# Kernel tuning notes

Hardware: AMD Instinct MI355X
Metric: run time of the kernel (lower is better)

## Reference

```python
import jax, jax.numpy as jnp
import numpy as np

N_SKILLS = 1000
N_PROBLEMS = 20000
EMB = 256
TIME_LOG = 5.0
B, S = 32, 2048


def setup_inputs() -> dict:
    key = jax.random.key(0)
    ks = jax.random.split(key, 10)
    skills = jax.random.randint(ks[0], (B, S), 0, N_SKILLS, dtype=jnp.int64) if jax.config.jax_enable_x64 else jax.random.randint(ks[0], (B, S), 0, N_SKILLS, dtype=jnp.int32)
    problems = jax.random.randint(ks[1], (B, S), 0, N_PROBLEMS, dtype=skills.dtype)
    times = jnp.sort(jax.random.randint(ks[2], (B, S), 0, 10_000_000, dtype=skills.dtype), axis=-1)
    labels = jax.random.randint(ks[3], (B, S), 0, 2, dtype=skills.dtype)
    std = 0.01
    alpha_inter_W = std * jax.random.normal(ks[4], (2 * N_SKILLS, EMB), dtype=jnp.float32)
    alpha_skill_W = std * jax.random.normal(ks[5], (N_SKILLS, EMB), dtype=jnp.float32)
    beta_inter_W = std * jax.random.normal(ks[6], (2 * N_SKILLS, EMB), dtype=jnp.float32)
    beta_skill_W = std * jax.random.normal(ks[7], (N_SKILLS, EMB), dtype=jnp.float32)
    problem_base_W = std * jax.random.normal(ks[8], (N_PROBLEMS, 1), dtype=jnp.float32)
    skill_base_W = std * jax.random.normal(ks[9], (N_SKILLS, 1), dtype=jnp.float32)
    return {
        "skills": skills, "problems": problems, "times": times, "labels": labels,
        "alpha_inter_W": alpha_inter_W, "alpha_skill_W": alpha_skill_W,
        "beta_inter_W": beta_inter_W, "beta_skill_W": beta_skill_W,
        "problem_base_W": problem_base_W, "skill_base_W": skill_base_W,
    }


def reference(skills, problems, times, labels,
              alpha_inter_W, alpha_skill_W, beta_inter_W, beta_skill_W,
              problem_base_W, skill_base_W):
    n_skills = alpha_skill_W.shape[0]
    inters = skills + labels * n_skills  # [B,S]

    alpha_src = alpha_inter_W[inters]      # [B,S,E]
    alpha_tgt = alpha_skill_W[skills]      # [B,S,E]
    alphas = jnp.einsum("bse,bte->bst", alpha_src, alpha_tgt)  # [B,S,S]

    beta_src = beta_inter_W[inters]
    beta_tgt = beta_skill_W[skills]
    betas = jnp.einsum("bse,bte->bst", beta_src, beta_tgt)
    betas = jnp.clip(betas + 1.0, 0.0, 10.0)

    t = times.astype(jnp.float32) / 1000.0
    delta_t = jnp.abs(t[:, :, None] - t[:, None, :])
    delta_t = jnp.log(delta_t + 1e-10) / jnp.log(jnp.float32(TIME_LOG))

    cross = alphas * jnp.exp(-betas * delta_t)  # [B,S,S]

    seq_len = skills.shape[1]
    # original keeps strict upper triangle (source i strictly before target j)
    keep = jnp.triu(jnp.ones((seq_len, seq_len), dtype=cross.dtype), k=1)
    sum_t = jnp.sum(cross * keep[None], axis=-2)  # sum over source dim -> [B,S]

    problem_bias = problem_base_W[problems][..., 0]  # [B,S]
    skill_bias = skill_base_W[skills][..., 0]        # [B,S]
    h = problem_bias + skill_bias + sum_t
    return jax.nn.sigmoid(h)
```

## Files before the change

kernel.cpp:

```cpp
#include <hip/hip_runtime.h>
#include <hip/hip_bf16.h>
#include <stdint.h>

#define NSK   1000
#define EMB   256
#define BB    32
#define SS    2048
#define TI    128
#define TJ    64
#define NUNITB 272
#define BK    64
#define NCHUNK (EMB / BK)
#define LDSB  24576
#define SCALE_INV (1.0f / 4096.0f)
#define LOG5I 0.6213349345596119f

typedef float f32x16 __attribute__((ext_vector_type(16)));
typedef float f32x4  __attribute__((ext_vector_type(4)));
typedef long  longx2 __attribute__((ext_vector_type(2)));
typedef int   i32x8  __attribute__((ext_vector_type(8)));

#define OFF_AI8 0
#define OFF_BI8 (2 * NSK * EMB)
#define OFF_AS8 (4 * NSK * EMB)
#define OFF_BS8 (5 * NSK * EMB)
#define TOT8    (6 * NSK * EMB)

__global__ void cvt_tables(const float* __restrict__ ai, const float* __restrict__ bi,
                           const float* __restrict__ as_, const float* __restrict__ bs,
                           int* __restrict__ ws8, float* __restrict__ acc) {
    int g = blockIdx.x * 256 + threadIdx.x;
    if (g < BB * SS) acc[g] = 0.0f;
    if (g * 4 >= TOT8) return;
    int e = g * 4;
    const float* src; int off;
    if (e < OFF_AS8) { if (e < OFF_BI8) { src = ai;  off = e; }
                       else             { src = bi;  off = e - OFF_BI8; } }
    else             { if (e < OFF_BS8) { src = as_; off = e - OFF_AS8; }
                       else             { src = bs;  off = e - OFF_BS8; } }
    const float4 v = *(const float4*)(src + off);
    int lo = __builtin_amdgcn_cvt_pk_fp8_f32(v.x * 64.0f, v.y * 64.0f, 0, false);
    int wd = __builtin_amdgcn_cvt_pk_fp8_f32(v.z * 64.0f, v.w * 64.0f, lo, true);
    ws8[g] = wd;
}

__device__ __attribute__((noinline)) float dot256(const float* __restrict__ a,
                                                  const float* __restrict__ b) {
    float s = 0.0f;
#pragma unroll 8
    for (int k = 0; k < EMB; ++k) s += a[k] * b[k];
    return s;
}

__global__ __launch_bounds__(256, 3) void hawkes_unit(
    const int* __restrict__ skills, const int* __restrict__ times,
    const int* __restrict__ labels, const unsigned char* __restrict__ tab,
    const float* __restrict__ aiW_f, const float* __restrict__ asW_f,
    const float* __restrict__ biW_f, const float* __restrict__ bsW_f,
    float* __restrict__ acc)
{
    __shared__ __align__(16) char  sbuf[2 * LDSB];
    __shared__ __align__(16) float t_i[TI];
    __shared__ __align__(16) float t_j[TJ];
    __shared__ int   idx_i[TI];
    __shared__ int   idx_j[TJ];
    __shared__ float colsum[TJ];

    const int u  = blockIdx.x;
    const int b  = u / NUNITB;
    const int p  = u - b * NUNITB;
    int m = (int)sqrtf((float)p);
    while ((m + 1) * (m + 2) <= p) ++m;
    while (m * (m + 1) > p) --m;
    int jt, it;
    if (p >= (m + 1) * (m + 1)) { jt = 2 * m + 1; it = p - (m + 1) * (m + 1); }
    else                        { jt = 2 * m;     it = p - m * (m + 1); }
    const int j0 = jt * TJ, i0 = it * TI;
    const bool partial = (i0 + TI - 1 >= j0);

    const int tid = threadIdx.x;
    const int l   = tid & 63;
    const int w   = tid >> 6;
    const int wi  = w >> 1, wj = w & 1;
    const int lane31 = l & 31;
    const int khalf  = l >> 5;

    if (tid < TJ) {
        int j = j0 + tid;
        idx_j[tid] = skills[b * SS + j];
        t_j[tid]   = (float)times[b * SS + j] / 1000.0f;
        colsum[tid] = 0.0f;
    } else if (tid < TJ + TI) {
        int q = tid - TJ;
        int ii = i0 + q;
        idx_i[q] = skills[b * SS + ii] + labels[b * SS + ii] * NSK;
        t_i[q]   = (float)times[b * SS + ii] / 1000.0f;
    }
    __syncthreads();

    const float tjv = t_j[wj * 32 + lane31];
    const int   jl  = wj * 32 + lane31;

    const unsigned char* rowptr[3];
    int wo[3];
#pragma unroll
    for (int s = 0; s < 3; ++s) {
        int mm = w * 3 + s;
        int tabbase, ldsbase, row;
        if (mm < 8) {
            int mb = mm & 3;
            tabbase = (mm < 4) ? OFF_AI8 : OFF_BI8;
            ldsbase = ((mm < 4) ? 0 : 8192) + mb * 2048;
            row = idx_i[mb * 32 + (l >> 1)];
        } else {
            int mb = mm & 1;
            tabbase = (mm < 10) ? OFF_AS8 : OFF_BS8;
            ldsbase = ((mm < 10) ? 16384 : 20480) + mb * 2048;
            row = idx_j[mb * 32 + (l >> 1)];
        }
        rowptr[s] = tab + tabbase + (size_t)row * EMB + (l & 1) * 32;
        wo[s] = ldsbase + (l & 1) * 1024 + (l >> 1) * 8;
    }

#define LOADC(dst, c)                                                  \
    do { _Pragma("unroll")                                             \
        for (int s = 0; s < 3; ++s) {                                  \
            dst[s][0] = *(const longx2*)(rowptr[s] + (c) * BK);        \
            dst[s][1] = *(const longx2*)(rowptr[s] + (c) * BK + 16);   \
        }                                                              \
    } while (0)
#define WRITEC(src, buf)                                               \
    do { char* db = sbuf + (buf) * LDSB;                               \
        _Pragma("unroll")                                              \
        for (int s = 0; s < 3; ++s) {                                  \
            *(long*)(db + wo[s])             = src[s][0].x;            \
            *(long*)(db + wo[s] + 256)       = src[s][0].y;            \
            *(long*)(db + wo[s] + 512)       = src[s][1].x;            \
            *(long*)(db + wo[s] + 512 + 256) = src[s][1].y;            \
        }                                                              \
    } while (0)

    f32x16 accA[2], accB[2];
#pragma unroll
    for (int mi = 0; mi < 2; ++mi) { accA[mi] = 0.0f; accB[mi] = 0.0f; }

    longx2 sreg[3][2];
    LOADC(sreg, 0);
    WRITEC(sreg, 0);

    union U8 { long l[4]; i32x8 v; };

    for (int c = 0; c < NCHUNK; ++c) {
        if (c + 1 < NCHUNK) LOADC(sreg, c + 1);
        __syncthreads();

        const char* sb = sbuf + (c & 1) * LDSB;
        {
            U8 F0, F1, G;
#pragma unroll
            for (int q = 0; q < 4; ++q) {
                const int qoff = (khalf * 2 + (q >> 1)) * 512 + (q & 1) * 256 + lane31 * 8;
                F0.l[q] = *(const long*)(sb + 0 + (wi * 2 + 0) * 2048 + qoff);
                F1.l[q] = *(const long*)(sb + 0 + (wi * 2 + 1) * 2048 + qoff);
                G.l[q]  = *(const long*)(sb + 16384 + wj * 2048 + qoff);
            }
            accA[0] = __builtin_amdgcn_mfma_scale_f32_32x32x64_f8f6f4(
                F0.v, G.v, accA[0], 0, 0, 0, 127, 0, 127);
            accA[1] = __builtin_amdgcn_mfma_scale_f32_32x32x64_f8f6f4(
                F1.v, G.v, accA[1], 0, 0, 0, 127, 0, 127);
        }
        {
            U8 F0, F1, G;
#pragma unroll
            for (int q = 0; q < 4; ++q) {
                const int qoff = (khalf * 2 + (q >> 1)) * 512 + (q & 1) * 256 + lane31 * 8;
                F0.l[q] = *(const long*)(sb + 8192 + (wi * 2 + 0) * 2048 + qoff);
                F1.l[q] = *(const long*)(sb + 8192 + (wi * 2 + 1) * 2048 + qoff);
                G.l[q]  = *(const long*)(sb + 20480 + wj * 2048 + qoff);
            }
            accB[0] = __builtin_amdgcn_mfma_scale_f32_32x32x64_f8f6f4(
                F0.v, G.v, accB[0], 0, 0, 0, 127, 0, 127);
            accB[1] = __builtin_amdgcn_mfma_scale_f32_32x32x64_f8f6f4(
                F1.v, G.v, accB[1], 0, 0, 0, 127, 0, 127);
        }

        if (c + 1 < NCHUNK) WRITEC(sreg, (c + 1) & 1);
    }

    float csum0 = 0.0f, csum1 = 0.0f;
    float dmin = 1.0f;
#pragma unroll
    for (int mi = 0; mi < 2; ++mi) {
        const int rbase = (wi * 2 + mi) * 32 + 4 * khalf;
        f32x4 tiv[4];
#pragma unroll
        for (int q = 0; q < 4; ++q) tiv[q] = *(const f32x4*)(t_i + rbase + 8 * q);
        if (!partial) {
#pragma unroll
            for (int r = 0; r < 16; ++r) {
                const int q = r >> 2, e = r & 3;
                float d  = fabsf(tiv[q][e] - tjv);
                float lg = __builtin_amdgcn_logf(d);
                lg = (d == 0.0f) ? 1.0e38f : lg;
                dmin = fminf(dmin, d);
                float bp  = __builtin_fmaf(accB[mi][r], SCALE_INV * LOG5I, LOG5I);
                float wgt = __builtin_amdgcn_exp2f(-bp * lg);
                if (r & 1) csum1 = __builtin_fmaf(accA[mi][r], wgt, csum1);
                else       csum0 = __builtin_fmaf(accA[mi][r], wgt, csum0);
            }
        } else {
#pragma unroll
            for (int r = 0; r < 16; ++r) {
                const int q = r >> 2, e = r & 3;
                const int il = rbase + 8 * q + e;
                const bool live = (i0 + il < j0 + jl);
                float d  = fabsf(tiv[q][e] - tjv);
                float lg = __builtin_amdgcn_logf(d);
                lg = (d == 0.0f) ? 1.0e38f : lg;
                dmin = live ? fminf(dmin, d) : dmin;
                float bp  = __builtin_fmaf(accB[mi][r], SCALE_INV * LOG5I, LOG5I);
                float a   = live ? accA[mi][r] : 0.0f;
                float wgt = __builtin_amdgcn_exp2f(-bp * lg);
                if (r & 1) csum1 = __builtin_fmaf(a, wgt, csum1);
                else       csum0 = __builtin_fmaf(a, wgt, csum0);
            }
        }
    }
    float csum = csum0 + csum1;

    if (__any(dmin == 0.0f)) {
        const float dl0 = __builtin_amdgcn_logf(1e-10f) * LOG5I;
        for (int mi = 0; mi < 2; ++mi) {
            const int rbase = (wi * 2 + mi) * 32 + 4 * khalf;
            for (int r = 0; r < 16; ++r) {
                const int il = rbase + 8 * (r >> 2) + (r & 3);
                if (partial && i0 + il >= j0 + jl) continue;
                if (fabsf(t_i[il] - tjv) == 0.0f) {
                    float alpha = dot256(aiW_f + (size_t)idx_i[il] * EMB,
                                         asW_f + (size_t)idx_j[jl] * EMB) * 4096.0f;
                    float braw  = dot256(biW_f + (size_t)idx_i[il] * EMB,
                                         bsW_f + (size_t)idx_j[jl] * EMB) * 4096.0f;
                    float beta = braw * SCALE_INV + 1.0f;
                    csum += alpha * __builtin_amdgcn_exp2f(-beta * dl0);
                }
            }
        }
    }
    csum *= SCALE_INV;

    __syncthreads();
    csum += __shfl_xor(csum, 32);
    if (l < 32)
        atomicAdd(&colsum[wj * 32 + lane31], csum);
    __syncthreads();
    if (tid < TJ)
        atomicAdd(&acc[b * SS + j0 + tid], colsum[tid]);
}

__global__ void hawkes_final(const int* __restrict__ skills, const int* __restrict__ problems,
                             const float* __restrict__ pbW, const float* __restrict__ sbW,
                             float* __restrict__ out) {
    int i = blockIdx.x * 256 + threadIdx.x;
    if (i >= BB * SS) return;
    float h = pbW[problems[i]] + sbW[skills[i]] + out[i];
    out[i] = 1.0f / (1.0f + __builtin_amdgcn_exp2f(-h * 1.4426950408889634f));
}

extern "C" void kernel_launch(void* const* d_in, const int* in_sizes, int n_in,
                              void* d_out, int out_size, void* d_ws, size_t ws_size,
                              hipStream_t stream) {
    const int*   skills   = (const int*)d_in[0];
    const int*   problems = (const int*)d_in[1];
    const int*   times    = (const int*)d_in[2];
    const int*   labels   = (const int*)d_in[3];
    const float* aiW      = (const float*)d_in[4];
    const float* asW      = (const float*)d_in[5];
    const float* biW      = (const float*)d_in[6];
    const float* bsW      = (const float*)d_in[7];
    const float* pbW      = (const float*)d_in[8];
    const float* sbW      = (const float*)d_in[9];
    float* out = (float*)d_out;
    unsigned char* tab = (unsigned char*)d_ws;

    cvt_tables<<<(TOT8 / 4 + 255) / 256, 256, 0, stream>>>(aiW, biW, asW, bsW,
                                                           (int*)tab, out);
    hawkes_unit<<<BB * NUNITB, 256, 0, stream>>>(skills, times, labels, tab,
                                                 aiW, asW, biW, bsW, out);
    hawkes_final<<<(BB * SS + 255) / 256, 256, 0, stream>>>(skills, problems, pbW, sbW, out);
}
```

Baseline: 164.0 us.

## Stage fp8 embedding tiles via direct global-to-LDS loads with new fragment layout

Replaces the register-staged global load plus LDS store of the fp8 embedding rows with the global_load_lds builtin (16 bytes per lane), writing straight into the double-buffered LDS tile. The LDS layout changes so each MFMA fragment is read with two 16-byte LDS loads instead of four 8-byte ones. This is meant to cut VGPR pressure and the LDS write instructions, and to overlap the next chunk's fetch with compute. It relies on the implicit lane-contiguous LDS placement of global_load_lds matching the new fragment offsets, and on the existing barrier being enough to order the asynchronous LDS writes.

```diff
diff --git a/kernel.cpp b/kernel.cpp
--- a/kernel.cpp
+++ b/kernel.cpp
@@ -52,6 +52,12 @@
     return s;
 }
 
+#define GLL(gp, lp)                                                        \
+    __builtin_amdgcn_global_load_lds(                                      \
+        (const __attribute__((address_space(1))) unsigned int*)(const void*)(gp), \
+        (__attribute__((address_space(3))) unsigned int*)(void*)(lp),      \
+        16, 0, 0)
+
 __global__ __launch_bounds__(256, 3) void hawkes_unit(
     const int* __restrict__ skills, const int* __restrict__ times,
     const int* __restrict__ labels, const unsigned char* __restrict__ tab,
@@ -101,8 +107,8 @@
     const float tjv = t_j[wj * 32 + lane31];
     const int   jl  = wj * 32 + lane31;
 
-    const unsigned char* rowptr[3];
-    int wo[3];
+    const unsigned char* rowbase[3];
+    int ldso[3];
 #pragma unroll
     for (int s = 0; s < 3; ++s) {
         int mm = w * 3 + s;
@@ -111,32 +117,23 @@
             int mb = mm & 3;
             tabbase = (mm < 4) ? OFF_AI8 : OFF_BI8;
             ldsbase = ((mm < 4) ? 0 : 8192) + mb * 2048;
-            row = idx_i[mb * 32 + (l >> 1)];
+            row = idx_i[mb * 32 + lane31];
         } else {
             int mb = mm & 1;
             tabbase = (mm < 10) ? OFF_AS8 : OFF_BS8;
             ldsbase = ((mm < 10) ? 16384 : 20480) + mb * 2048;
-            row = idx_j[mb * 32 + (l >> 1)];
-        }
-        rowptr[s] = tab + tabbase + (size_t)row * EMB + (l & 1) * 32;
-        wo[s] = ldsbase + (l & 1) * 1024 + (l >> 1) * 8;
-    }
-
-#define LOADC(dst, c)                                                  \
-    do { _Pragma("unroll")                                             \
-        for (int s = 0; s < 3; ++s) {                                  \
-            dst[s][0] = *(const longx2*)(rowptr[s] + (c) * BK);        \
-            dst[s][1] = *(const longx2*)(rowptr[s] + (c) * BK + 16);   \
-        }                                                              \
-    } while (0)
-#define WRITEC(src, buf)                                               \
+            row = idx_j[mb * 32 + lane31];
+        }
+        rowbase[s] = tab + tabbase + (size_t)row * EMB + khalf * 16;
+        ldso[s] = ldsbase;
+    }
+
+#define GSTAGE(c, buf)                                                 \
     do { char* db = sbuf + (buf) * LDSB;                               \
         _Pragma("unroll")                                              \
         for (int s = 0; s < 3; ++s) {                                  \
-            *(long*)(db + wo[s])             = src[s][0].x;            \
-            *(long*)(db + wo[s] + 256)       = src[s][0].y;            \
-            *(long*)(db + wo[s] + 512)       = src[s][1].x;            \
-            *(long*)(db + wo[s] + 512 + 256) = src[s][1].y;            \
+            GLL(rowbase[s] + (c) * BK,      db + ldso[s]);             \
+            GLL(rowbase[s] + (c) * BK + 32, db + ldso[s] + 1024);      \
         }                                                              \
     } while (0)
 
@@ -144,26 +141,27 @@
 #pragma unroll
     for (int mi = 0; mi < 2; ++mi) { accA[mi] = 0.0f; accB[mi] = 0.0f; }
 
-    longx2 sreg[3][2];
-    LOADC(sreg, 0);
-    WRITEC(sreg, 0);
+    GSTAGE(0, 0);
 
     union U8 { long l[4]; i32x8 v; };
+    const int fro = khalf * 1024 + lane31 * 16;
+
+#define RDFRAG(dst, base)                                              \
+    do { longx2 t0 = *(const longx2*)((base) + fro);                   \
+         longx2 t1 = *(const longx2*)((base) + fro + 512);             \
+         dst.l[0] = t0.x; dst.l[1] = t0.y;                             \
+         dst.l[2] = t1.x; dst.l[3] = t1.y; } while (0)
 
     for (int c = 0; c < NCHUNK; ++c) {
-        if (c + 1 < NCHUNK) LOADC(sreg, c + 1);
         __syncthreads();
+        if (c + 1 < NCHUNK) GSTAGE(c + 1, (c + 1) & 1);
 
         const char* sb = sbuf + (c & 1) * LDSB;
         {
             U8 F0, F1, G;
-#pragma unroll
-            for (int q = 0; q < 4; ++q) {
-                const int qoff = (khalf * 2 + (q >> 1)) * 512 + (q & 1) * 256 + lane31 * 8;
-                F0.l[q] = *(const long*)(sb + 0 + (wi * 2 + 0) * 2048 + qoff);
-                F1.l[q] = *(const long*)(sb + 0 + (wi * 2 + 1) * 2048 + qoff);
-                G.l[q]  = *(const long*)(sb + 16384 + wj * 2048 + qoff);
-            }
+            RDFRAG(F0, sb + 0 + (wi * 2 + 0) * 2048);
+            RDFRAG(F1, sb + 0 + (wi * 2 + 1) * 2048);
+            RDFRAG(G,  sb + 16384 + wj * 2048);
             accA[0] = __builtin_amdgcn_mfma_scale_f32_32x32x64_f8f6f4(
                 F0.v, G.v, accA[0], 0, 0, 0, 127, 0, 127);
             accA[1] = __builtin_amdgcn_mfma_scale_f32_32x32x64_f8f6f4(
@@ -171,20 +169,14 @@
         }
         {
             U8 F0, F1, G;
-#pragma unroll
-            for (int q = 0; q < 4; ++q) {
-                const int qoff = (khalf * 2 + (q >> 1)) * 512 + (q & 1) * 256 + lane31 * 8;
-                F0.l[q] = *(const long*)(sb + 8192 + (wi * 2 + 0) * 2048 + qoff);
-                F1.l[q] = *(const long*)(sb + 8192 + (wi * 2 + 1) * 2048 + qoff);
-                G.l[q]  = *(const long*)(sb + 20480 + wj * 2048 + qoff);
-            }
+            RDFRAG(F0, sb + 8192 + (wi * 2 + 0) * 2048);
+            RDFRAG(F1, sb + 8192 + (wi * 2 + 1) * 2048);
+            RDFRAG(G,  sb + 20480 + wj * 2048);
             accB[0] = __builtin_amdgcn_mfma_scale_f32_32x32x64_f8f6f4(
                 F0.v, G.v, accB[0], 0, 0, 0, 127, 0, 127);
             accB[1] = __builtin_amdgcn_mfma_scale_f32_32x32x64_f8f6f4(
                 F1.v, G.v, accB[1], 0, 0, 0, 127, 0, 127);
         }
-
-        if (c + 1 < NCHUNK) WRITEC(sreg, (c + 1) & 1);
     }
 
     float csum0 = 0.0f, csum1 = 0.0f;
```

New measurement: 195.2 us. 19.0% more time.
